# Kernel optimization log

Measured on AMD Instinct MI355X. Metric: run time of the kernel, lower is better.

## Reference

```python
import jax, jax.numpy as jnp
import numpy as np

N_NODES = 50000
N_GRAPHS = 128
IN_DIM = 512
HID = 512
N_LAYERS = 3


def setup_inputs() -> dict:
    key = jax.random.key(0)
    ks = jax.random.split(key, 12)
    inp = {
        "x": jax.random.normal(ks[0], (N_NODES, IN_DIM), dtype=jnp.float32),
        "walk2": jax.random.randint(ks[1], (3, N_NODES), 0, N_NODES, dtype=jnp.int32),
        "walk3": jax.random.randint(ks[2], (4, N_NODES), 0, N_NODES, dtype=jnp.int32),
        "walk4": jax.random.randint(ks[3], (5, N_NODES), 0, N_NODES, dtype=jnp.int32),
        "batch": jnp.sort(jax.random.randint(ks[4], (N_NODES,), 0, N_GRAPHS, dtype=jnp.int32)),
    }
    dims = [IN_DIM, HID, HID]
    for i in range(N_LAYERS):
        scale = 1.0 / np.sqrt(dims[i])
        inp[f"W{i}"] = jax.random.normal(ks[5 + i], (dims[i], HID), dtype=jnp.float32) * scale
        inp[f"b{i}"] = jnp.zeros((HID,), dtype=jnp.float32)
    return inp


def _gather_sum(z, walk):
    # walk: [L, N] node indices -> sum of gathered embeddings, [N, H]
    L, N = walk.shape
    return jnp.take(z, walk.reshape(-1), axis=0).reshape(L, N, z.shape[1]).sum(0)


def reference(x, walk2, walk3, walk4, batch, W0, b0, W1, b1, W2, b2):
    layers = [(W0, b0), (W1, b1), (W2, b2)]
    path_batch = jnp.take(batch, walk2[0])  # [N]
    counts = jax.ops.segment_sum(jnp.ones((path_batch.shape[0],), jnp.float32),
                                 path_batch, num_segments=N_GRAPHS)
    denom = jnp.maximum(counts, 1.0)[:, None]  # avoid div-by-zero for empty graphs
    z = x
    g = []
    for W, b in layers:
        z = z @ W + b  # [N, H]
        path_emb = _gather_sum(z, walk2) + _gather_sum(z, walk3) + _gather_sum(z, walk4)
        pooled = jax.ops.segment_sum(path_emb, path_batch, num_segments=N_GRAPHS) / denom
        g.append(pooled)
    return jnp.concatenate(g, axis=1)  # [N_GRAPHS, 3*H]
```

## Files before the change

### kernel.cpp

```cpp
#include <hip/hip_runtime.h>

#define N_NODES 50000
#define N_GRAPHS 128
#define HID 512

#define KSPLIT 128
#define KSPAN  416
#define KPAD   (KSPLIT * KSPAN)
#define C8_BYTES  ((size_t)N_GRAPHS * KPAD)
#define PSUM_OFF  C8_BYTES
#define COUNTS_OFF (PSUM_OFF + (size_t)N_GRAPHS * HID * 4)
#define ZERO_BYTES (COUNTS_OFF + 512)
#define PART_OFF  ZERO_BYTES
#define PART_BYTES ((size_t)KSPLIT * N_GRAPHS * HID * 4)

typedef __attribute__((ext_vector_type(8))) short bf16x8;
typedef __attribute__((ext_vector_type(16))) float f32x16;

struct U4 { uint2 a, b; };

__global__ __launch_bounds__(256)
void build_c_kernel(const int* __restrict__ w2, const int* __restrict__ w3,
                    const int* __restrict__ w4, const int* __restrict__ batch,
                    unsigned int* __restrict__ C32, int* __restrict__ counts) {
    __shared__ int hist[N_GRAPHS];
    const int t = threadIdx.x;
    if (t < N_GRAPHS) hist[t] = 0;
    __syncthreads();
    const int i = blockIdx.x * 256 + t;
    if (i < N_NODES) {
        const int a = w2[i];
        const int g = batch[a];
        atomicAdd(&hist[g], 1);
        unsigned int* row = C32 + (size_t)g * (KPAD / 4);
        int nn[12];
        nn[0]  = a;
        nn[1]  = w2[N_NODES + i];
        nn[2]  = w2[2 * N_NODES + i];
        nn[3]  = w3[i];
        nn[4]  = w3[N_NODES + i];
        nn[5]  = w3[2 * N_NODES + i];
        nn[6]  = w3[3 * N_NODES + i];
        nn[7]  = w4[i];
        nn[8]  = w4[N_NODES + i];
        nn[9]  = w4[2 * N_NODES + i];
        nn[10] = w4[3 * N_NODES + i];
        nn[11] = w4[4 * N_NODES + i];
#pragma unroll
        for (int j = 0; j < 12; ++j) {
            const int nd = nn[j];
            atomicAdd(&row[nd >> 2], 1u << ((nd & 3) * 8));
        }
    }
    __syncthreads();
    if (t < N_GRAPHS) { const int hv = hist[t]; if (hv) atomicAdd(&counts[t], hv); }
}

__device__ inline bf16x8 cnt_frag(uint2 v) {
    bf16x8 r;
#pragma unroll
    for (int j = 0; j < 4; ++j) {
        r[j]     = (short)(__builtin_bit_cast(unsigned, (float)((v.x >> (8 * j)) & 0xFFu)) >> 16);
        r[4 + j] = (short)(__builtin_bit_cast(unsigned, (float)((v.y >> (8 * j)) & 0xFFu)) >> 16);
    }
    return r;
}

template <int ATOMIC>
__global__ __launch_bounds__(512, 4)
void pool_gemm_kernel(const float* __restrict__ x,
                      const unsigned char* __restrict__ C8,
                      float* __restrict__ dst) {
    __shared__ unsigned int BH[128 * 18];
    __shared__ unsigned int BL[128 * 18];

    const int nt = blockIdx.x;
    const int ks = blockIdx.y;
    const int t = threadIdx.x;
    const int lane = t & 63;
    const int w = t >> 6;
    const int ns = w & 3;
    const int mh = w >> 2;
    const int n = lane & 31;
    const int h = lane >> 5;

    const int colbase = nt * 128;
    const int c = t & 127;
    const int strip = t >> 7;

    const unsigned char* arow0 = C8 + (size_t)(mh * 64 + n) * KPAD;
    const unsigned char* arow1 = arow0 + (size_t)32 * KPAD;

    f32x16 acc0, acc1;
#pragma unroll
    for (int i = 0; i < 16; ++i) { acc0[i] = 0.f; acc1[i] = 0.f; }

    for (int ch = 0; ch < KSPAN / 32; ++ch) {
        const int k0 = ks * KSPAN + ch * 32;

        const int aoff = k0 + h * 8;
        const uint2 a00 = *(const uint2*)(arow0 + aoff);
        const uint2 a01 = *(const uint2*)(arow0 + aoff + 16);
        const uint2 a10 = *(const uint2*)(arow1 + aoff);
        const uint2 a11 = *(const uint2*)(arow1 + aoff + 16);

        const int kb = k0 + strip * 8;
        float v[8];
#pragma unroll
        for (int j = 0; j < 8; ++j) {
            const int k = kb + j;
            v[j] = (k < N_NODES) ? x[(size_t)k * HID + colbase + c] : 0.f;
        }
        unsigned hw[4], lw[4];
#pragma unroll
        for (int j = 0; j < 4; ++j) {
            const unsigned u0 = __builtin_bit_cast(unsigned, v[2 * j]);
            const unsigned u1 = __builtin_bit_cast(unsigned, v[2 * j + 1]);
            const unsigned h0 = u0 & 0xFFFF0000u, h1 = u1 & 0xFFFF0000u;
            hw[j] = (h0 >> 16) | h1;
            const float r0 = v[2 * j] - __builtin_bit_cast(float, h0);
            const float r1 = v[2 * j + 1] - __builtin_bit_cast(float, h1);
            lw[j] = (__builtin_bit_cast(unsigned, r0) >> 16) |
                    (__builtin_bit_cast(unsigned, r1) & 0xFFFF0000u);
        }
        __syncthreads();
        const int widx = c * 18 + strip * 4;
        *(uint2*)&BH[widx]     = make_uint2(hw[0], hw[1]);
        *(uint2*)&BH[widx + 2] = make_uint2(hw[2], hw[3]);
        *(uint2*)&BL[widx]     = make_uint2(lw[0], lw[1]);
        *(uint2*)&BL[widx + 2] = make_uint2(lw[2], lw[3]);
        __syncthreads();

#pragma unroll
        for (int kk = 0; kk < 2; ++kk) {
            const int bidx = (ns * 32 + n) * 18 + kk * 8 + h * 4;
            U4 uh, ul;
            uh.a = *(const uint2*)&BH[bidx];
            uh.b = *(const uint2*)&BH[bidx + 2];
            ul.a = *(const uint2*)&BL[bidx];
            ul.b = *(const uint2*)&BL[bidx + 2];
            const bf16x8 bh = __builtin_bit_cast(bf16x8, uh);
            const bf16x8 bl = __builtin_bit_cast(bf16x8, ul);
            const bf16x8 af0 = cnt_frag(kk ? a01 : a00);
            const bf16x8 af1 = cnt_frag(kk ? a11 : a10);
            acc0 = __builtin_amdgcn_mfma_f32_32x32x16_bf16(af0, bh, acc0, 0, 0, 0);
            acc1 = __builtin_amdgcn_mfma_f32_32x32x16_bf16(af1, bh, acc1, 0, 0, 0);
            acc0 = __builtin_amdgcn_mfma_f32_32x32x16_bf16(af0, bl, acc0, 0, 0, 0);
            acc1 = __builtin_amdgcn_mfma_f32_32x32x16_bf16(af1, bl, acc1, 0, 0, 0);
        }
    }

    const int col = colbase + ns * 32 + n;
    float* outp = ATOMIC ? dst : dst + (size_t)ks * N_GRAPHS * HID;
#pragma unroll
    for (int r = 0; r < 16; ++r) {
        const int row0 = mh * 64 + (r & 3) + 8 * (r >> 2) + 4 * h;
        if (ATOMIC) {
            atomicAdd(&outp[(size_t)row0 * HID + col], acc0[r]);
            atomicAdd(&outp[(size_t)(row0 + 32) * HID + col], acc1[r]);
        } else {
            outp[(size_t)row0 * HID + col] = acc0[r];
            outp[(size_t)(row0 + 32) * HID + col] = acc1[r];
        }
    }
}

__global__ __launch_bounds__(256)
void reduce_part_kernel(const float* __restrict__ part, float* __restrict__ Psum) {
    const int id = blockIdx.x * 256 + threadIdx.x;
    float s0 = 0.f, s1 = 0.f, s2 = 0.f, s3 = 0.f;
    for (int s = 0; s < KSPLIT; s += 4) {
        s0 += part[(size_t)s * (N_GRAPHS * HID) + id];
        s1 += part[(size_t)(s + 1) * (N_GRAPHS * HID) + id];
        s2 += part[(size_t)(s + 2) * (N_GRAPHS * HID) + id];
        s3 += part[(size_t)(s + 3) * (N_GRAPHS * HID) + id];
    }
    Psum[id] = (s0 + s1) + (s2 + s3);
}

__global__ __launch_bounds__(256)
void layer_gemm_kernel(const float* __restrict__ A, int lda, int scaleA,
                       const float* __restrict__ W,
                       const float* __restrict__ bias,
                       const int* __restrict__ counts,
                       float* __restrict__ out) {
    __shared__ float Alds[16][128];
    const int ct = blockIdx.x, rt = blockIdx.y, ksb = blockIdx.z;
    const int t = threadIdx.x;
    const int cc = ct * 64 + (t & 63);
    const int wv = t >> 6;
    const int k0 = ksb * 128;

    for (int idx = t; idx < 16 * 32; idx += 256) {
        const int rr = idx >> 5;
        const int kk = (idx & 31) * 4;
        const int row = rt * 16 + rr;
        float4 v = *(const float4*)&A[(size_t)row * lda + k0 + kk];
        if (scaleA) {
            const float inv = 1.f / (float)max(counts[row], 1);
            v.x *= inv; v.y *= inv; v.z *= inv; v.w *= inv;
        }
        *(float4*)&Alds[rr][kk] = v;
    }
    __syncthreads();

    const int r0 = rt * 16 + wv * 4;
    float a0 = 0.f, a1 = 0.f, a2 = 0.f, a3 = 0.f;
#pragma unroll 8
    for (int k = 0; k < 128; ++k) {
        const float wval = W[(size_t)(k0 + k) * HID + cc];
        a0 += Alds[wv * 4 + 0][k] * wval;
        a1 += Alds[wv * 4 + 1][k] * wval;
        a2 += Alds[wv * 4 + 2][k] * wval;
        a3 += Alds[wv * 4 + 3][k] * wval;
    }
    if (ksb == 0) {
        const float bc = bias[cc];
        a0 += (counts[r0 + 0] > 0 ? 12.f : 0.f) * bc;
        a1 += (counts[r0 + 1] > 0 ? 12.f : 0.f) * bc;
        a2 += (counts[r0 + 2] > 0 ? 12.f : 0.f) * bc;
        a3 += (counts[r0 + 3] > 0 ? 12.f : 0.f) * bc;
    }
    atomicAdd(&out[(size_t)(r0 + 0) * 1536 + cc], a0);
    atomicAdd(&out[(size_t)(r0 + 1) * 1536 + cc], a1);
    atomicAdd(&out[(size_t)(r0 + 2) * 1536 + cc], a2);
    atomicAdd(&out[(size_t)(r0 + 3) * 1536 + cc], a3);
}

extern "C" void kernel_launch(void* const* d_in, const int* in_sizes, int n_in,
                              void* d_out, int out_size, void* d_ws, size_t ws_size,
                              hipStream_t stream) {
    const float* x     = (const float*)d_in[0];
    const int*   w2    = (const int*)d_in[1];
    const int*   w3    = (const int*)d_in[2];
    const int*   w4    = (const int*)d_in[3];
    const int*   batch = (const int*)d_in[4];
    const float* W0    = (const float*)d_in[5];
    const float* b0    = (const float*)d_in[6];
    const float* W1    = (const float*)d_in[7];
    const float* b1    = (const float*)d_in[8];
    const float* W2    = (const float*)d_in[9];
    const float* b2    = (const float*)d_in[10];
    float* out = (float*)d_out;

    unsigned char* ws = (unsigned char*)d_ws;
    unsigned int* C32 = (unsigned int*)ws;
    float* Psum = (float*)(ws + PSUM_OFF);
    int* counts = (int*)(ws + COUNTS_OFF);
    float* part = (float*)(ws + PART_OFF);
    const bool use_part = ws_size >= PART_OFF + PART_BYTES;

    hipMemsetAsync(d_ws, 0, ZERO_BYTES, stream);
    hipMemsetAsync(d_out, 0, (size_t)out_size * 4, stream);

    build_c_kernel<<<(N_NODES + 255) / 256, 256, 0, stream>>>(w2, w3, w4, batch, C32, counts);

    if (use_part) {
        pool_gemm_kernel<0><<<dim3(4, KSPLIT), 512, 0, stream>>>(x, ws, part);
        reduce_part_kernel<<<256, 256, 0, stream>>>(part, Psum);
    } else {
        pool_gemm_kernel<1><<<dim3(4, KSPLIT), 512, 0, stream>>>(x, ws, Psum);
    }

    layer_gemm_kernel<<<dim3(8, 8, 4), 256, 0, stream>>>(Psum, HID, 1, W0, b0, counts, out);
    layer_gemm_kernel<<<dim3(8, 8, 4), 256, 0, stream>>>(out, 1536, 0, W1, b1, counts, out + 512);
    layer_gemm_kernel<<<dim3(8, 8, 4), 256, 0, stream>>>(out + 512, 1536, 0, W2, b2, counts, out + 1024);
}
```

Before: 273.2 us.

## Pre-convert count matrix to bf16 and restructure pooling GEMM without LDS

Adds a separate kernel that expands the 8-bit count matrix into bf16 once, so the pooling GEMM loads ready-made A fragments instead of converting them in its inner loop. The pooling GEMM is rewritten so each wave owns 64 columns and all 128 graph rows (4x2 MFMA tiles). B fragments are loaded straight from global memory into registers, which drops the LDS staging and both barriers. The K split changes to 241 chunks of 208. This costs an extra conversion pass, a larger workspace, more partial sums to reduce, and higher register pressure.

```diff
diff --git a/kernel.cpp b/kernel.cpp
--- a/kernel.cpp
+++ b/kernel.cpp
@@ -4,20 +4,23 @@
 #define N_GRAPHS 128
 #define HID 512
 
-#define KSPLIT 128
-#define KSPAN  416
-#define KPAD   (KSPLIT * KSPAN)
-#define C8_BYTES  ((size_t)N_GRAPHS * KPAD)
-#define PSUM_OFF  C8_BYTES
-#define COUNTS_OFF (PSUM_OFF + (size_t)N_GRAPHS * HID * 4)
+#define KSPAN  208
+#define KSPLIT 241
+#define KPAD   (KSPAN * KSPLIT)
+
+#define C8_OFF     0
+#define C8_BYTES   ((size_t)N_GRAPHS * KPAD)
+#define PSUM_OFF   (C8_OFF + C8_BYTES)
+#define PSUM_BYTES ((size_t)N_GRAPHS * HID * 4)
+#define COUNTS_OFF (PSUM_OFF + PSUM_BYTES)
 #define ZERO_BYTES (COUNTS_OFF + 512)
-#define PART_OFF  ZERO_BYTES
+#define CBF_OFF    ZERO_BYTES
+#define CBF_BYTES  (2 * C8_BYTES)
+#define PART_OFF   (CBF_OFF + CBF_BYTES)
 #define PART_BYTES ((size_t)KSPLIT * N_GRAPHS * HID * 4)
 
 typedef __attribute__((ext_vector_type(8))) short bf16x8;
 typedef __attribute__((ext_vector_type(16))) float f32x16;
-
-struct U4 { uint2 a, b; };
 
 __global__ __launch_bounds__(256)
 void build_c_kernel(const int* __restrict__ w2, const int* __restrict__ w3,
@@ -56,125 +59,130 @@
     if (t < N_GRAPHS) { const int hv = hist[t]; if (hv) atomicAdd(&counts[t], hv); }
 }
 
-__device__ inline bf16x8 cnt_frag(uint2 v) {
-    bf16x8 r;
+__global__ __launch_bounds__(256)
+void c8_to_bf16_kernel(const unsigned int* __restrict__ C32,
+                       unsigned int* __restrict__ Cbf) {
+    const int i = blockIdx.x * 256 + threadIdx.x;
+    const int total = N_GRAPHS * (KPAD / 4);
+    if (i >= total) return;
+    const unsigned v = C32[i];
+    const float f0 = (float)(v & 0xFFu);
+    const float f1 = (float)((v >> 8) & 0xFFu);
+    const float f2 = (float)((v >> 16) & 0xFFu);
+    const float f3 = (float)(v >> 24);
+    Cbf[2 * i]     = (__builtin_bit_cast(unsigned, f0) >> 16) |
+                     (__builtin_bit_cast(unsigned, f1) & 0xFFFF0000u);
+    Cbf[2 * i + 1] = (__builtin_bit_cast(unsigned, f2) >> 16) |
+                     (__builtin_bit_cast(unsigned, f3) & 0xFFFF0000u);
+}
+
+template <int GUARD>
+__device__ inline void make_b(const float* __restrict__ x, int k0, int h,
+                              int col, bf16x8& bh, bf16x8& bl) {
+    float v[8];
+#pragma unroll
+    for (int j = 0; j < 8; ++j) {
+        const int k = k0 + 8 * h + j;
+        v[j] = (!GUARD || k < N_NODES) ? x[(size_t)k * HID + col] : 0.f;
+    }
+    unsigned hw[4], lw[4];
 #pragma unroll
     for (int j = 0; j < 4; ++j) {
-        r[j]     = (short)(__builtin_bit_cast(unsigned, (float)((v.x >> (8 * j)) & 0xFFu)) >> 16);
-        r[4 + j] = (short)(__builtin_bit_cast(unsigned, (float)((v.y >> (8 * j)) & 0xFFu)) >> 16);
-    }
-    return r;
+        const unsigned u0 = __builtin_bit_cast(unsigned, v[2 * j]);
+        const unsigned u1 = __builtin_bit_cast(unsigned, v[2 * j + 1]);
+        const unsigned h0 = u0 & 0xFFFF0000u, h1 = u1 & 0xFFFF0000u;
+        hw[j] = (h0 >> 16) | h1;
+        const float r0 = v[2 * j] - __builtin_bit_cast(float, h0);
+        const float r1 = v[2 * j + 1] - __builtin_bit_cast(float, h1);
+        lw[j] = (__builtin_bit_cast(unsigned, r0) >> 16) |
+                (__builtin_bit_cast(unsigned, r1) & 0xFFFF0000u);
+    }
+    uint4 uh = make_uint4(hw[0], hw[1], hw[2], hw[3]);
+    uint4 ul = make_uint4(lw[0], lw[1], lw[2], lw[3]);
+    bh = __builtin_bit_cast(bf16x8, uh);
+    bl = __builtin_bit_cast(bf16x8, ul);
 }
 
 template <int ATOMIC>
-__global__ __launch_bounds__(512, 4)
-void pool_gemm_kernel(const float* __restrict__ x,
-                      const unsigned char* __restrict__ C8,
-                      float* __restrict__ dst) {
-    __shared__ unsigned int BH[128 * 18];
-    __shared__ unsigned int BL[128 * 18];
-
-    const int nt = blockIdx.x;
-    const int ks = blockIdx.y;
+__global__ __launch_bounds__(256, 2)
+void pool_gemm2_kernel(const float* __restrict__ x,
+                       const unsigned int* __restrict__ Cbf,
+                       float* __restrict__ dst) {
     const int t = threadIdx.x;
     const int lane = t & 63;
     const int w = t >> 6;
-    const int ns = w & 3;
-    const int mh = w >> 2;
     const int n = lane & 31;
     const int h = lane >> 5;
-
-    const int colbase = nt * 128;
-    const int c = t & 127;
-    const int strip = t >> 7;
-
-    const unsigned char* arow0 = C8 + (size_t)(mh * 64 + n) * KPAD;
-    const unsigned char* arow1 = arow0 + (size_t)32 * KPAD;
-
-    f32x16 acc0, acc1;
-#pragma unroll
-    for (int i = 0; i < 16; ++i) { acc0[i] = 0.f; acc1[i] = 0.f; }
-
-    for (int ch = 0; ch < KSPAN / 32; ++ch) {
-        const int k0 = ks * KSPAN + ch * 32;
-
-        const int aoff = k0 + h * 8;
-        const uint2 a00 = *(const uint2*)(arow0 + aoff);
-        const uint2 a01 = *(const uint2*)(arow0 + aoff + 16);
-        const uint2 a10 = *(const uint2*)(arow1 + aoff);
-        const uint2 a11 = *(const uint2*)(arow1 + aoff + 16);
-
-        const int kb = k0 + strip * 8;
-        float v[8];
-#pragma unroll
-        for (int j = 0; j < 8; ++j) {
-            const int k = kb + j;
-            v[j] = (k < N_NODES) ? x[(size_t)k * HID + colbase + c] : 0.f;
-        }
-        unsigned hw[4], lw[4];
-#pragma unroll
-        for (int j = 0; j < 4; ++j) {
-            const unsigned u0 = __builtin_bit_cast(unsigned, v[2 * j]);
-            const unsigned u1 = __builtin_bit_cast(unsigned, v[2 * j + 1]);
-            const unsigned h0 = u0 & 0xFFFF0000u, h1 = u1 & 0xFFFF0000u;
-            hw[j] = (h0 >> 16) | h1;
-            const float r0 = v[2 * j] - __builtin_bit_cast(float, h0);
-            const float r1 = v[2 * j + 1] - __builtin_bit_cast(float, h1);
-            lw[j] = (__builtin_bit_cast(unsigned, r0) >> 16) |
-                    (__builtin_bit_cast(unsigned, r1) & 0xFFFF0000u);
-        }
-        __syncthreads();
-        const int widx = c * 18 + strip * 4;
-        *(uint2*)&BH[widx]     = make_uint2(hw[0], hw[1]);
-        *(uint2*)&BH[widx + 2] = make_uint2(hw[2], hw[3]);
-        *(uint2*)&BL[widx]     = make_uint2(lw[0], lw[1]);
-        *(uint2*)&BL[widx + 2] = make_uint2(lw[2], lw[3]);
-        __syncthreads();
-
-#pragma unroll
-        for (int kk = 0; kk < 2; ++kk) {
-            const int bidx = (ns * 32 + n) * 18 + kk * 8 + h * 4;
-            U4 uh, ul;
-            uh.a = *(const uint2*)&BH[bidx];
-            uh.b = *(const uint2*)&BH[bidx + 2];
-            ul.a = *(const uint2*)&BL[bidx];
-            ul.b = *(const uint2*)&BL[bidx + 2];
-            const bf16x8 bh = __builtin_bit_cast(bf16x8, uh);
-            const bf16x8 bl = __builtin_bit_cast(bf16x8, ul);
-            const bf16x8 af0 = cnt_frag(kk ? a01 : a00);
-            const bf16x8 af1 = cnt_frag(kk ? a11 : a10);
-            acc0 = __builtin_amdgcn_mfma_f32_32x32x16_bf16(af0, bh, acc0, 0, 0, 0);
-            acc1 = __builtin_amdgcn_mfma_f32_32x32x16_bf16(af1, bh, acc1, 0, 0, 0);
-            acc0 = __builtin_amdgcn_mfma_f32_32x32x16_bf16(af0, bl, acc0, 0, 0, 0);
-            acc1 = __builtin_amdgcn_mfma_f32_32x32x16_bf16(af1, bl, acc1, 0, 0, 0);
-        }
-    }
-
-    const int col = colbase + ns * 32 + n;
-    float* outp = ATOMIC ? dst : dst + (size_t)ks * N_GRAPHS * HID;
-#pragma unroll
-    for (int r = 0; r < 16; ++r) {
-        const int row0 = mh * 64 + (r & 3) + 8 * (r >> 2) + 4 * h;
-        if (ATOMIC) {
-            atomicAdd(&outp[(size_t)row0 * HID + col], acc0[r]);
-            atomicAdd(&outp[(size_t)(row0 + 32) * HID + col], acc1[r]);
+    const int colbase = (blockIdx.x * 4 + w) * 64;
+    const int ks = blockIdx.y;
+    const int kbase = ks * KSPAN;
+
+    f32x16 acc[4][2];
+#pragma unroll
+    for (int mt = 0; mt < 4; ++mt)
+#pragma unroll
+        for (int nt = 0; nt < 2; ++nt)
+#pragma unroll
+            for (int r = 0; r < 16; ++r) acc[mt][nt][r] = 0.f;
+
+    const int col0 = colbase + n;
+
+    for (int s = 0; s < KSPAN / 16; ++s) {
+        const int k0 = kbase + s * 16;
+
+        bf16x8 af[4];
+#pragma unroll
+        for (int mt = 0; mt < 4; ++mt) {
+            const unsigned int* ap =
+                Cbf + (size_t)(mt * 32 + n) * (KPAD / 2) + (unsigned)(k0 + 8 * h) / 2;
+            af[mt] = __builtin_bit_cast(bf16x8, *(const uint4*)ap);
+        }
+
+        bf16x8 bh0, bl0, bh1, bl1;
+        if (k0 + 16 <= N_NODES) {
+            make_b<0>(x, k0, h, col0, bh0, bl0);
+            make_b<0>(x, k0, h, col0 + 32, bh1, bl1);
         } else {
-            outp[(size_t)row0 * HID + col] = acc0[r];
-            outp[(size_t)(row0 + 32) * HID + col] = acc1[r];
-        }
-    }
+            make_b<1>(x, k0, h, col0, bh0, bl0);
+            make_b<1>(x, k0, h, col0 + 32, bh1, bl1);
+        }
+
+#pragma unroll
+        for (int mt = 0; mt < 4; ++mt) {
+            acc[mt][0] = __builtin_amdgcn_mfma_f32_32x32x16_bf16(af[mt], bh0, acc[mt][0], 0, 0, 0);
+            acc[mt][0] = __builtin_amdgcn_mfma_f32_32x32x16_bf16(af[mt], bl0, acc[mt][0], 0, 0, 0);
+            acc[mt][1] = __builtin_amdgcn_mfma_f32_32x32x16_bf16(af[mt], bh1, acc[mt][1], 0, 0, 0);
+            acc[mt][1] = __builtin_amdgcn_mfma_f32_32x32x16_bf16(af[mt], bl1, acc[mt][1], 0, 0, 0);
+        }
+    }
+
+    float* outp = ATOMIC ? dst : dst + (size_t)ks * (N_GRAPHS * HID);
+#pragma unroll
+    for (int mt = 0; mt < 4; ++mt)
+#pragma unroll
+        for (int nt = 0; nt < 2; ++nt) {
+            const int col = colbase + nt * 32 + n;
+#pragma unroll
+            for (int r = 0; r < 16; ++r) {
+                const int row = mt * 32 + (r & 3) + 8 * (r >> 2) + 4 * h;
+                if (ATOMIC) atomicAdd(&outp[(size_t)row * HID + col], acc[mt][nt][r]);
+                else        outp[(size_t)row * HID + col] = acc[mt][nt][r];
+            }
+        }
 }
 
 __global__ __launch_bounds__(256)
 void reduce_part_kernel(const float* __restrict__ part, float* __restrict__ Psum) {
     const int id = blockIdx.x * 256 + threadIdx.x;
     float s0 = 0.f, s1 = 0.f, s2 = 0.f, s3 = 0.f;
-    for (int s = 0; s < KSPLIT; s += 4) {
-        s0 += part[(size_t)s * (N_GRAPHS * HID) + id];
-        s1 += part[(size_t)(s + 1) * (N_GRAPHS * HID) + id];
-        s2 += part[(size_t)(s + 2) * (N_GRAPHS * HID) + id];
-        s3 += part[(size_t)(s + 3) * (N_GRAPHS * HID) + id];
-    }
+    int k = 0;
+    for (; k + 4 <= KSPLIT; k += 4) {
+        s0 += part[(size_t)k * (N_GRAPHS * HID) + id];
+        s1 += part[(size_t)(k + 1) * (N_GRAPHS * HID) + id];
+        s2 += part[(size_t)(k + 2) * (N_GRAPHS * HID) + id];
+        s3 += part[(size_t)(k + 3) * (N_GRAPHS * HID) + id];
+    }
+    for (; k < KSPLIT; ++k) s0 += part[(size_t)k * (N_GRAPHS * HID) + id];
     Psum[id] = (s0 + s1) + (s2 + s3);
 }
 
@@ -244,10 +252,11 @@
     float* out = (float*)d_out;
 
     unsigned char* ws = (unsigned char*)d_ws;
-    unsigned int* C32 = (unsigned int*)ws;
-    float* Psum = (float*)(ws + PSUM_OFF);
-    int* counts = (int*)(ws + COUNTS_OFF);
-    float* part = (float*)(ws + PART_OFF);
+    unsigned int* C32 = (unsigned int*)(ws + C8_OFF);
+    float* Psum       = (float*)(ws + PSUM_OFF);
+    int* counts       = (int*)(ws + COUNTS_OFF);
+    unsigned int* Cbf = (unsigned int*)(ws + CBF_OFF);
+    float* part       = (float*)(ws + PART_OFF);
     const bool use_part = ws_size >= PART_OFF + PART_BYTES;
 
     hipMemsetAsync(d_ws, 0, ZERO_BYTES, stream);
@@ -255,11 +264,14 @@
 
     build_c_kernel<<<(N_NODES + 255) / 256, 256, 0, stream>>>(w2, w3, w4, batch, C32, counts);
 
+    const int cvt_total = N_GRAPHS * (KPAD / 4);
+    c8_to_bf16_kernel<<<(cvt_total + 255) / 256, 256, 0, stream>>>(C32, Cbf);
+
     if (use_part) {
-        pool_gemm_kernel<0><<<dim3(4, KSPLIT), 512, 0, stream>>>(x, ws, part);
+        pool_gemm2_kernel<0><<<dim3(2, KSPLIT), 256, 0, stream>>>(x, Cbf, part);
         reduce_part_kernel<<<256, 256, 0, stream>>>(part, Psum);
     } else {
-        pool_gemm_kernel<1><<<dim3(4, KSPLIT), 512, 0, stream>>>(x, ws, Psum);
+        pool_gemm2_kernel<1><<<dim3(2, KSPLIT), 256, 0, stream>>>(x, Cbf, Psum);
     }
 
     layer_gemm_kernel<<<dim3(8, 8, 4), 256, 0, stream>>>(Psum, HID, 1, W0, b0, counts, out);
```

After: 289.7 us. 6.0% more time.
